# Performance work log

Hardware: AMD Instinct MI355X
Metric: run time of the kernel (lower is better)

The kernel has to match this reference:

```python
import jax, jax.numpy as jnp
import numpy as np


def setup_inputs() -> dict:
    key = jax.random.key(0)
    k1, k2, k3, k4 = jax.random.split(key, 4)
    N, F_in, F_out = 8192, 512, 256
    inp = jax.random.normal(k1, (N, F_in), dtype=jnp.float32)
    adj = jax.random.uniform(k2, (N, N), dtype=jnp.float32)
    stdv = 1.0 / np.sqrt(F_out)
    weight = jax.random.uniform(k3, (F_in, F_out), minval=-stdv, maxval=stdv, dtype=jnp.float32)
    b = jax.random.uniform(k4, (F_out,), minval=-stdv, maxval=stdv, dtype=jnp.float32)
    return {"input": inp, "adj": adj, "weight": weight, "b": b}


def reference(input, adj, weight, b):
    N = adj.shape[0]
    degree = jnp.sum(adj, axis=1)                      # [N]
    # A_tilde = 2*I - adj
    A_tilde = 2.0 * jnp.eye(N, dtype=adj.dtype) - adj
    d_inv_sqrt = 1.0 / jnp.sqrt(2.0 + degree)          # [N]
    # D^-1/2 @ A_tilde @ D^-1/2 as broadcasted row/col scaling (same math, O(N^2))
    L_sharpen = d_inv_sqrt[:, None] * A_tilde * d_inv_sqrt[None, :]
    support = input @ weight                           # [N, F_out]
    out = L_sharpen @ support + b                      # [N, F_out]
    return jax.nn.relu(out)
```

## Files before the change

kernel.cpp:

```cpp
#include <hip/hip_runtime.h>


typedef _Float16 h4 __attribute__((ext_vector_type(4)));
typedef _Float16 h8 __attribute__((ext_vector_type(8)));
typedef float f4 __attribute__((ext_vector_type(4)));

__device__ __forceinline__ void gload_lds16(const void* g, void* l) {
    __builtin_amdgcn_global_load_lds(
        (const __attribute__((address_space(1))) void*)g,
        (__attribute__((address_space(3))) void*)l, 16, 0, 0);
}

__device__ __forceinline__ void gload2(const float* p, f4& x, f4& y) {
    asm volatile("global_load_dwordx4 %0, %2, off\n\t"
                 "global_load_dwordx4 %1, %2, off offset:16"
                 : "=&v"(x), "=&v"(y)
                 : "v"(p)
                 : "memory");
}
__device__ __forceinline__ void gloadBfrag(const char* p, h8& x, h8& y) {
    asm volatile("global_load_dwordx4 %0, %2, off\n\t"
                 "global_load_dwordx4 %1, %2, off offset:1024"
                 : "=&v"(x), "=&v"(y)
                 : "v"(p)
                 : "memory");
}

__global__ __launch_bounds__(256) void k0_wt(const float* __restrict__ weight,
                                             char* __restrict__ wt) {
    const int idx = blockIdx.x * 256 + threadIdx.x;
    const int k = idx >> 8, j = idx & 255;
    const _Float16 h = (_Float16)weight[idx];
    const int off = j * 1024 + ((k >> 6) << 7) + (((k & 63) << 1) ^ ((j & 7) << 4));
    *(_Float16*)(wt + off) = h;
}

__global__ __launch_bounds__(256) void k1_deg(const float* __restrict__ adj,
                                              float* __restrict__ dinv) {
    const int r = blockIdx.x;
    const float4* rp = (const float4*)(adj + (size_t)r * 8192);
    const int t = threadIdx.x;
    float s = 0.f;
#pragma unroll
    for (int i = 0; i < 8; ++i) {
        float4 v = rp[t + i * 256];
        s += (v.x + v.y) + (v.z + v.w);
    }
#pragma unroll
    for (int off = 32; off > 0; off >>= 1) s += __shfl_down(s, off, 64);
    __shared__ float part[4];
    if ((t & 63) == 0) part[t >> 6] = s;
    __syncthreads();
    if (t == 0) {
        float deg = (part[0] + part[1]) + (part[2] + part[3]);
        dinv[r] = 1.0f / sqrtf(2.0f + deg);
    }
}

__global__ __launch_bounds__(512) void k2_support(const float* __restrict__ input,
                                                  const char* __restrict__ wt,
                                                  const float* __restrict__ dinv,
                                                  char* __restrict__ sT) {
    __shared__ char smem[4096 + 32768];
    const int t = threadIdx.x, w = t >> 6, l = t & 63;
    const int r0 = (int)blockIdx.x * 32;
    const int arow = t >> 4, ak4 = t & 15;
    const int bj = l >> 3, bb = (l & 7) * 16;

    f4 acc[2][2] = {};

    for (int kt = 0; kt < 8; ++kt) {
        const int k0 = kt * 64;
        __syncthreads();
        {
            float4 v = *(const float4*)(input + (size_t)(r0 + arow) * 512 + k0 + ak4 * 4);
            h4 h;
            h[0] = (_Float16)v.x; h[1] = (_Float16)v.y;
            h[2] = (_Float16)v.z; h[3] = (_Float16)v.w;
            *(h4*)(smem + arow * 128 + ((ak4 * 8) ^ ((arow & 7) << 4))) = h;
        }
#pragma unroll
        for (int q = 0; q < 4; ++q) {
            const int c = q * 8 + w;
            gload_lds16(wt + (size_t)(c * 8 + bj) * 1024 + kt * 128 + bb,
                        smem + 4096 + c * 1024);
        }
        __syncthreads();
#pragma unroll
        for (int kk = 0; kk < 2; ++kk) {
            const int ko = kk * 64 + ((l >> 4) << 4);
            h8 a[2], b[2];
#pragma unroll
            for (int m = 0; m < 2; ++m) {
                const int r = m * 16 + (l & 15);
                a[m] = *(const h8*)(smem + r * 128 + (ko ^ ((r & 7) << 4)));
            }
#pragma unroll
            for (int n = 0; n < 2; ++n) {
                const int j = w * 32 + n * 16 + (l & 15);
                b[n] = *(const h8*)(smem + 4096 + j * 128 + (ko ^ ((j & 7) << 4)));
            }
#pragma unroll
            for (int m = 0; m < 2; ++m)
#pragma unroll
                for (int n = 0; n < 2; ++n)
                    acc[m][n] = __builtin_amdgcn_mfma_f32_16x16x32_f16(a[m], b[n], acc[m][n], 0, 0, 0);
        }
    }
#pragma unroll
    for (int m = 0; m < 2; ++m)
#pragma unroll
        for (int n = 0; n < 2; ++n) {
            const int j = w * 32 + n * 16 + (l & 15);
            const int k0r = r0 + m * 16 + ((l >> 4) << 2);
            h4 h;
#pragma unroll
            for (int r = 0; r < 4; ++r)
                h[r] = (_Float16)(dinv[k0r + r] * acc[m][n][r]);
            const int off = (((j >> 4) * 128 + (k0r >> 6)) << 11) +
                            (((k0r >> 5) & 1) << 10) +
                            ((((k0r >> 3) & 3) << 4) + (j & 15)) * 16 +
                            ((k0r & 7) << 1);
            *(h4*)(sT + off) = h;
        }
}

__global__ __launch_bounds__(512, 4) void k3_spmm(const float* __restrict__ adj,
                                                  const char* __restrict__ sT,
                                                  float* __restrict__ part,
                                                  float* __restrict__ out,
                                                  int steps) {
    __shared__ __align__(16) char smem[2][8192];
    const int t = threadIdx.x;
    const int w = t >> 6, l = t & 63;
    const int i0 = (int)blockIdx.x * 64;
    const int ks0 = (int)blockIdx.y * steps * 64;
    const int dkt = (i0 - ks0) >> 6;

    const int arow = t >> 3;
    const int ak8 = (t & 7) * 8;
    const int arow_g = i0 + arow;
    const float* aptr = adj + (size_t)arow_g * 8192 + ks0 + ak8;
    const int a_off = arow * 128 + (((t & 7) << 4) ^ ((arow & 7) << 4));

    const int chunk0 = ks0 >> 6;
    const char* bpn0 = sT + ((size_t)(w * 2) * 128 + chunk0) * 2048 + l * 16;
    const char* bpn1 = bpn0 + 262144;

    f4 acc[4][2] = {};
    h8 bvA[2][2], bvB[2][2];
    f4 ax0, ay0, ax1, ay1;

    auto loadB = [&](int kt, h8 (&bv)[2][2]) {
        gloadBfrag(bpn0 + (size_t)kt * 2048, bv[0][0], bv[1][0]);
        gloadBfrag(bpn1 + (size_t)kt * 2048, bv[0][1], bv[1][1]);
    };
    auto writeA = [&](char* buf, int kt, const f4 x, const f4 y) {
        const int kg = ks0 + kt * 64 + ak8;
        h8 h;
        if (kt == dkt) {
#pragma unroll
            for (int e = 0; e < 4; ++e)
                h[e] = (_Float16)((arow_g == kg + e) ? 2.0f - x[e] : -x[e]);
#pragma unroll
            for (int e = 0; e < 4; ++e)
                h[4 + e] = (_Float16)((arow_g == kg + 4 + e) ? 2.0f - y[e] : -y[e]);
        } else {
#pragma unroll
            for (int e = 0; e < 4; ++e) h[e] = (_Float16)(-x[e]);
#pragma unroll
            for (int e = 0; e < 4; ++e) h[4 + e] = (_Float16)(-y[e]);
        }
        *(h8*)(buf + a_off) = h;
    };
    auto compute = [&](const char* A, const h8 (&bv)[2][2]) {
#pragma unroll
        for (int kk = 0; kk < 2; ++kk) {
            const int ko = kk * 64 + ((l >> 4) << 4);
            h8 a[4];
#pragma unroll
            for (int m = 0; m < 4; ++m) {
                const int r = m * 16 + (l & 15);
                a[m] = *(const h8*)(A + r * 128 + (ko ^ ((r & 7) << 4)));
            }
#pragma unroll
            for (int m = 0; m < 4; ++m)
#pragma unroll
                for (int n = 0; n < 2; ++n)
                    acc[m][n] = __builtin_amdgcn_mfma_f32_16x16x32_f16(a[m], bv[kk][n], acc[m][n], 0, 0, 0);
        }
    };

#define SBAR0() __builtin_amdgcn_sched_barrier(0)
#define WAIT_ADJ(N, X, Y)                                                     \
    asm volatile("s_waitcnt vmcnt(" #N ")" : "+v"(X), "+v"(Y) :: "memory");   \
    SBAR0();
#define WAIT_STEP(N, X, Y, BV)                                                \
    asm volatile("s_waitcnt vmcnt(" #N ")"                                    \
                 : "+v"(X), "+v"(Y), "+v"(BV[0][0]), "+v"(BV[0][1]),          \
                   "+v"(BV[1][0]), "+v"(BV[1][1]) :: "memory");               \
    SBAR0();
#define WAIT_BV(N, BV)                                                        \
    asm volatile("s_waitcnt vmcnt(" #N ")"                                    \
                 : "+v"(BV[0][0]), "+v"(BV[0][1]),                            \
                   "+v"(BV[1][0]), "+v"(BV[1][1]) :: "memory");               \
    SBAR0();
#define BARRIER()                                                             \
    asm volatile("s_waitcnt lgkmcnt(0)\n\ts_barrier" ::: "memory");           \
    SBAR0();

    gload2(aptr, ax0, ay0);
    loadB(0, bvA);
    WAIT_ADJ(4, ax0, ay0)
    writeA(smem[0], 0, ax0, ay0);
    gload2(aptr + 64, ax1, ay1);
    BARRIER()

#define BODY(kt, XC, YC, XN, YN, BVC, BVN, BUFC, BUFN)                        \
    {                                                                         \
        loadB((kt) + 1, BVN);                                                 \
        gload2(aptr + (size_t)((kt) + 2) * 64, XC, YC);                       \
        WAIT_STEP(6, XN, YN, BVC)                                             \
        writeA(BUFN, (kt) + 1, XN, YN);                                       \
        compute(BUFC, BVC);                                                   \
        BARRIER()                                                             \
    }

    for (int kt2 = 0; kt2 + 2 <= steps - 2; kt2 += 2) {
        BODY(kt2,     ax0, ay0, ax1, ay1, bvA, bvB, smem[0], smem[1])
        BODY(kt2 + 1, ax1, ay1, ax0, ay0, bvB, bvA, smem[1], smem[0])
    }
    {
        loadB(steps - 1, bvB);
        WAIT_STEP(4, ax1, ay1, bvA)
        writeA(smem[1], steps - 1, ax1, ay1);
        compute(smem[0], bvA);
        BARRIER()
    }
    {
        WAIT_BV(0, bvB)
        compute(smem[1], bvB);
    }
#undef BODY
#undef WAIT_ADJ
#undef WAIT_STEP
#undef WAIT_BV
#undef BARRIER
#undef SBAR0

    float* dst = (blockIdx.y == gridDim.y - 1) ? out
               : part + (size_t)blockIdx.y * (8192 * 256);
#pragma unroll
    for (int m = 0; m < 4; ++m)
#pragma unroll
        for (int n = 0; n < 2; ++n) {
            const int j = w * 32 + n * 16 + (l & 15);
            const int ib = i0 + m * 16 + ((l >> 4) << 2);
#pragma unroll
            for (int r = 0; r < 4; ++r)
                dst[(size_t)(ib + r) * 256 + j] = acc[m][n][r];
        }
}

__global__ __launch_bounds__(256) void k4_fin(const float* __restrict__ part,
                                              float* __restrict__ out,
                                              const float* __restrict__ dinv,
                                              const float* __restrict__ bias,
                                              int nsplit) {
    const int idx = blockIdx.x * 256 + threadIdx.x;
    float4 s = ((const float4*)out)[idx];
    for (int sp = 0; sp < nsplit - 1; ++sp)
        s += ((const float4*)(part + (size_t)sp * (8192 * 256)))[idx];
    const float dv = dinv[idx >> 6];
    const float4 b = ((const float4*)bias)[idx & 63];
    float4 r;
    r.x = fmaxf(dv * s.x + b.x, 0.f);
    r.y = fmaxf(dv * s.y + b.y, 0.f);
    r.z = fmaxf(dv * s.z + b.z, 0.f);
    r.w = fmaxf(dv * s.w + b.w, 0.f);
    ((float4*)out)[idx] = r;
}

extern "C" void kernel_launch(void* const* d_in, const int* in_sizes, int n_in,
                              void* d_out, int out_size, void* d_ws, size_t ws_size,
                              hipStream_t stream) {
    const float* input  = (const float*)d_in[0];
    const float* adj    = (const float*)d_in[1];
    const float* weight = (const float*)d_in[2];
    const float* bias   = (const float*)d_in[3];
    float* out = (float*)d_out;

    char* ws = (char*)d_ws;
    float* dinv = (float*)ws;
    char*  wt   = ws + 32768;
    char*  sT   = ws + 294912;
    float* part = (float*)(ws + 294912 + 4194304);

    const size_t base = 294912 + 4194304;
    int nsplit = 1;
    if (ws_size >= base + 3 * 8388608) nsplit = 4;
    else if (ws_size >= base + 1 * 8388608) nsplit = 2;
    const int steps = 128 / nsplit;

    k0_wt<<<512, 256, 0, stream>>>(weight, wt);
    k1_deg<<<8192, 256, 0, stream>>>(adj, dinv);
    k2_support<<<256, 512, 0, stream>>>(input, wt, dinv, sT);
    k3_spmm<<<dim3(128, nsplit), 512, 0, stream>>>(adj, sT, part, out, steps);
    k4_fin<<<2048, 256, 0, stream>>>(part, out, dinv, bias, nsplit);
}
```

Baseline: 136.9 us.

## Widen SpMM K-tile to 256 with four sub-steps per barrier

Restructures the k3_spmm main loop so each LDS tile covers 256 columns of adj instead of 64. Each tile is processed in four 64-wide sub-steps, with B-fragment loads double-buffered across sub-steps and the next adj tile's loads interleaved between them. The goal is to need one workgroup barrier per 256 columns rather than per 64, and to keep more global loads in flight. In exchange LDS per block grows from 16 KB to 64 KB and more registers are live, which may reduce occupancy under launch_bounds(512,4).

```diff
diff --git a/kernel.cpp b/kernel.cpp
--- a/kernel.cpp
+++ b/kernel.cpp
@@ -130,58 +130,70 @@
                                                   float* __restrict__ part,
                                                   float* __restrict__ out,
                                                   int steps) {
-    __shared__ __align__(16) char smem[2][8192];
+    __shared__ __align__(16) char smem[2][32768];
     const int t = threadIdx.x;
     const int w = t >> 6, l = t & 63;
     const int i0 = (int)blockIdx.x * 64;
-    const int ks0 = (int)blockIdx.y * steps * 64;
-    const int dkt = (i0 - ks0) >> 6;
+    const int ks0 = (int)blockIdx.y * steps * 256;
+    const int ts_d = ((unsigned)(i0 - ks0) < (unsigned)(steps * 256))
+                     ? ((i0 - ks0) >> 8) : -1;
 
     const int arow = t >> 3;
-    const int ak8 = (t & 7) * 8;
+    const int ak16 = (t & 7) * 16;
     const int arow_g = i0 + arow;
-    const float* aptr = adj + (size_t)arow_g * 8192 + ks0 + ak8;
-    const int a_off = arow * 128 + (((t & 7) << 4) ^ ((arow & 7) << 4));
-
-    const int chunk0 = ks0 >> 6;
-    const char* bpn0 = sT + ((size_t)(w * 2) * 128 + chunk0) * 2048 + l * 16;
+    const float* aptr = adj + (size_t)arow_g * 8192 + ks0 + ak16;
+    const int aswz = (arow & 7) << 4;
+    const int abase = arow * 512;
+
+    const char* bpn0 = sT + ((size_t)(w * 2) * 128 + (ks0 >> 6)) * 2048 + l * 16;
     const char* bpn1 = bpn0 + 262144;
 
     f4 acc[4][2] = {};
     h8 bvA[2][2], bvB[2][2];
-    f4 ax0, ay0, ax1, ay1;
-
-    auto loadB = [&](int kt, h8 (&bv)[2][2]) {
-        gloadBfrag(bpn0 + (size_t)kt * 2048, bv[0][0], bv[1][0]);
-        gloadBfrag(bpn1 + (size_t)kt * 2048, bv[0][1], bv[1][1]);
+    f4 pa0, pa1, pa2, pa3;
+    f4 pb0, pb1, pb2, pb3;
+
+    auto loadB = [&](int s, h8 (&bv)[2][2]) {
+        gloadBfrag(bpn0 + (size_t)s * 2048, bv[0][0], bv[1][0]);
+        gloadBfrag(bpn1 + (size_t)s * 2048, bv[0][1], bv[1][1]);
     };
-    auto writeA = [&](char* buf, int kt, const f4 x, const f4 y) {
-        const int kg = ks0 + kt * 64 + ak8;
-        h8 h;
-        if (kt == dkt) {
-#pragma unroll
-            for (int e = 0; e < 4; ++e)
-                h[e] = (_Float16)((arow_g == kg + e) ? 2.0f - x[e] : -x[e]);
-#pragma unroll
-            for (int e = 0; e < 4; ++e)
-                h[4 + e] = (_Float16)((arow_g == kg + 4 + e) ? 2.0f - y[e] : -y[e]);
+    auto loadAr = [&](int tile, int r, f4& x0, f4& y0, f4& x1, f4& y1) {
+        const float* p = aptr + (size_t)tile * 256 + r * 128;
+        gload2(p, x0, y0);
+        gload2(p + 8, x1, y1);
+    };
+    auto writeAr = [&](char* buf, int tile, int r,
+                       const f4 x0, const f4 y0, const f4 x1, const f4 y1) {
+        h8 u, v;
+        if (tile == ts_d) {
+            const int kg = ks0 + tile * 256 + ak16 + r * 128;
+#pragma unroll
+            for (int e = 0; e < 4; ++e) {
+                u[e]     = (_Float16)((arow_g == kg + e     ) ? 2.0f - x0[e] : -x0[e]);
+                u[4 + e] = (_Float16)((arow_g == kg + 4 + e ) ? 2.0f - y0[e] : -y0[e]);
+                v[e]     = (_Float16)((arow_g == kg + 8 + e ) ? 2.0f - x1[e] : -x1[e]);
+                v[4 + e] = (_Float16)((arow_g == kg + 12 + e) ? 2.0f - y1[e] : -y1[e]);
+            }
         } else {
 #pragma unroll
-            for (int e = 0; e < 4; ++e) h[e] = (_Float16)(-x[e]);
-#pragma unroll
-            for (int e = 0; e < 4; ++e) h[4 + e] = (_Float16)(-y[e]);
-        }
-        *(h8*)(buf + a_off) = h;
+            for (int e = 0; e < 4; ++e) {
+                u[e] = (_Float16)(-x0[e]); u[4 + e] = (_Float16)(-y0[e]);
+                v[e] = (_Float16)(-x1[e]); v[4 + e] = (_Float16)(-y1[e]);
+            }
+        }
+        const int kb = (ak16 << 1) + r * 256;
+        *(h8*)(buf + abase + (kb ^ aswz)) = u;
+        *(h8*)(buf + abase + ((kb + 16) ^ aswz)) = v;
     };
-    auto compute = [&](const char* A, const h8 (&bv)[2][2]) {
+    auto compute = [&](const char* A, int sp, const h8 (&bv)[2][2]) {
 #pragma unroll
         for (int kk = 0; kk < 2; ++kk) {
-            const int ko = kk * 64 + ((l >> 4) << 4);
+            const int kb = sp * 128 + kk * 64 + ((l >> 4) << 4);
             h8 a[4];
 #pragma unroll
             for (int m = 0; m < 4; ++m) {
                 const int r = m * 16 + (l & 15);
-                a[m] = *(const h8*)(A + r * 128 + (ko ^ ((r & 7) << 4)));
+                a[m] = *(const h8*)(A + r * 512 + (kb ^ ((r & 7) << 4)));
             }
 #pragma unroll
             for (int m = 0; m < 4; ++m)
@@ -192,61 +204,78 @@
     };
 
 #define SBAR0() __builtin_amdgcn_sched_barrier(0)
-#define WAIT_ADJ(N, X, Y)                                                     \
-    asm volatile("s_waitcnt vmcnt(" #N ")" : "+v"(X), "+v"(Y) :: "memory");   \
-    SBAR0();
-#define WAIT_STEP(N, X, Y, BV)                                                \
-    asm volatile("s_waitcnt vmcnt(" #N ")"                                    \
-                 : "+v"(X), "+v"(Y), "+v"(BV[0][0]), "+v"(BV[0][1]),          \
-                   "+v"(BV[1][0]), "+v"(BV[1][1]) :: "memory");               \
-    SBAR0();
 #define WAIT_BV(N, BV)                                                        \
     asm volatile("s_waitcnt vmcnt(" #N ")"                                    \
                  : "+v"(BV[0][0]), "+v"(BV[0][1]),                            \
                    "+v"(BV[1][0]), "+v"(BV[1][1]) :: "memory");               \
     SBAR0();
+#define WAIT_BVA(N, BV, X0, Y0, X1, Y1)                                       \
+    asm volatile("s_waitcnt vmcnt(" #N ")"                                    \
+                 : "+v"(BV[0][0]), "+v"(BV[0][1]),                            \
+                   "+v"(BV[1][0]), "+v"(BV[1][1]),                            \
+                   "+v"(X0), "+v"(Y0), "+v"(X1), "+v"(Y1) :: "memory");       \
+    SBAR0();
 #define BARRIER()                                                             \
     asm volatile("s_waitcnt lgkmcnt(0)\n\ts_barrier" ::: "memory");           \
     SBAR0();
 
-    gload2(aptr, ax0, ay0);
+    loadAr(0, 0, pa0, pa1, pa2, pa3);
+    loadAr(0, 1, pb0, pb1, pb2, pb3);
     loadB(0, bvA);
-    WAIT_ADJ(4, ax0, ay0)
-    writeA(smem[0], 0, ax0, ay0);
-    gload2(aptr + 64, ax1, ay1);
+    asm volatile("s_waitcnt vmcnt(8)"
+                 : "+v"(pa0), "+v"(pa1), "+v"(pa2), "+v"(pa3) :: "memory");
+    SBAR0();
+    writeAr(smem[0], 0, 0, pa0, pa1, pa2, pa3);
+    asm volatile("s_waitcnt vmcnt(4)"
+                 : "+v"(pb0), "+v"(pb1), "+v"(pb2), "+v"(pb3) :: "memory");
+    SBAR0();
+    writeAr(smem[0], 0, 1, pb0, pb1, pb2, pb3);
     BARRIER()
 
-#define BODY(kt, XC, YC, XN, YN, BVC, BVN, BUFC, BUFN)                        \
-    {                                                                         \
-        loadB((kt) + 1, BVN);                                                 \
-        gload2(aptr + (size_t)((kt) + 2) * 64, XC, YC);                       \
-        WAIT_STEP(6, XN, YN, BVC)                                             \
-        writeA(BUFN, (kt) + 1, XN, YN);                                       \
-        compute(BUFC, BVC);                                                   \
-        BARRIER()                                                             \
-    }
-
-    for (int kt2 = 0; kt2 + 2 <= steps - 2; kt2 += 2) {
-        BODY(kt2,     ax0, ay0, ax1, ay1, bvA, bvB, smem[0], smem[1])
-        BODY(kt2 + 1, ax1, ay1, ax0, ay0, bvB, bvA, smem[1], smem[0])
+    for (int ts = 0; ts + 1 < steps; ++ts) {
+        char* AC = smem[ts & 1];
+        char* AN = smem[(ts & 1) ^ 1];
+        const int s0 = ts * 4;
+        loadB(s0 + 1, bvB);
+        WAIT_BV(4, bvA)
+        compute(AC, 0, bvA);
+
+        loadB(s0 + 2, bvA);
+        loadAr(ts + 1, 0, pa0, pa1, pa2, pa3);
+        WAIT_BV(8, bvB)
+        compute(AC, 1, bvB);
+
+        loadB(s0 + 3, bvB);
+        WAIT_BVA(4, bvA, pa0, pa1, pa2, pa3)
+        writeAr(AN, ts + 1, 0, pa0, pa1, pa2, pa3);
+        loadAr(ts + 1, 1, pb0, pb1, pb2, pb3);
+        compute(AC, 2, bvA);
+
+        loadB(s0 + 4, bvA);
+        WAIT_BVA(4, bvB, pb0, pb1, pb2, pb3)
+        writeAr(AN, ts + 1, 1, pb0, pb1, pb2, pb3);
+        compute(AC, 3, bvB);
+        BARRIER()
     }
     {
-        loadB(steps - 1, bvB);
-        WAIT_STEP(4, ax1, ay1, bvA)
-        writeA(smem[1], steps - 1, ax1, ay1);
-        compute(smem[0], bvA);
-        BARRIER()
-    }
-    {
+        const char* AC = smem[(steps - 1) & 1];
+        const int s0 = (steps - 1) * 4;
+        loadB(s0 + 1, bvB);
+        WAIT_BV(4, bvA)
+        compute(AC, 0, bvA);
+        loadB(s0 + 2, bvA);
+        WAIT_BV(4, bvB)
+        compute(AC, 1, bvB);
+        loadB(s0 + 3, bvB);
+        WAIT_BV(4, bvA)
+        compute(AC, 2, bvA);
         WAIT_BV(0, bvB)
-        compute(smem[1], bvB);
-    }
-#undef BODY
-#undef WAIT_ADJ
-#undef WAIT_STEP
+        compute(AC, 3, bvB);
+    }
+#undef SBAR0
 #undef WAIT_BV
+#undef WAIT_BVA
 #undef BARRIER
-#undef SBAR0
 
     float* dst = (blockIdx.y == gridDim.y - 1) ? out
                : part + (size_t)blockIdx.y * (8192 * 256);
@@ -300,7 +329,7 @@
     int nsplit = 1;
     if (ws_size >= base + 3 * 8388608) nsplit = 4;
     else if (ws_size >= base + 1 * 8388608) nsplit = 2;
-    const int steps = 128 / nsplit;
+    const int steps = 8192 / (nsplit * 256);
 
     k0_wt<<<512, 256, 0, stream>>>(weight, wt);
     k1_deg<<<8192, 256, 0, stream>>>(adj, dinv);
```

New measurement: 138.4 us. No clear change (+1.1%).

## Fuse split-K finalize into spmm via atomic counter and restructure degree kernel

Applied to the files above, without the earlier changes.

Removes the separate finalize kernel. Every split-K block of the spmm kernel now writes its partial sums to a workspace slot, bumps a per-row-tile atomic counter, and the last block to arrive sums all slots with cache-bypassing loads and applies the dinv scale, bias and ReLU. The degree kernel is rewritten so each half-wavefront handles one row, with 16 rows per block and 4 independent accumulators, to cut block count and reduction overhead. In exchange every split slot (including the last) is written out and then read back, and the workspace check changes so that only 4-way split or no split is selected.

```diff
diff --git a/kernel.cpp b/kernel.cpp
--- a/kernel.cpp
+++ b/kernel.cpp
@@ -10,51 +10,57 @@
         (const __attribute__((address_space(1))) void*)g,
         (__attribute__((address_space(3))) void*)l, 16, 0, 0);
 }
-
 __device__ __forceinline__ void gload2(const float* p, f4& x, f4& y) {
     asm volatile("global_load_dwordx4 %0, %2, off\n\t"
                  "global_load_dwordx4 %1, %2, off offset:16"
-                 : "=&v"(x), "=&v"(y)
-                 : "v"(p)
-                 : "memory");
+                 : "=&v"(x), "=&v"(y) : "v"(p) : "memory");
 }
 __device__ __forceinline__ void gloadBfrag(const char* p, h8& x, h8& y) {
     asm volatile("global_load_dwordx4 %0, %2, off\n\t"
                  "global_load_dwordx4 %1, %2, off offset:1024"
-                 : "=&v"(x), "=&v"(y)
-                 : "v"(p)
-                 : "memory");
+                 : "=&v"(x), "=&v"(y) : "v"(p) : "memory");
+}
+__device__ __forceinline__ f4 gloadSC(const float* p) {
+    f4 v;
+    asm volatile("global_load_dwordx4 %0, %1, off sc0 sc1\n\t"
+                 "s_waitcnt vmcnt(0)"
+                 : "=v"(v) : "v"(p) : "memory");
+    return v;
 }
 
 __global__ __launch_bounds__(256) void k0_wt(const float* __restrict__ weight,
-                                             char* __restrict__ wt) {
+                                             char* __restrict__ wt,
+                                             int* __restrict__ cnt) {
     const int idx = blockIdx.x * 256 + threadIdx.x;
     const int k = idx >> 8, j = idx & 255;
     const _Float16 h = (_Float16)weight[idx];
     const int off = j * 1024 + ((k >> 6) << 7) + (((k & 63) << 1) ^ ((j & 7) << 4));
     *(_Float16*)(wt + off) = h;
-}
-
-__global__ __launch_bounds__(256) void k1_deg(const float* __restrict__ adj,
+    if (blockIdx.x == 0 && threadIdx.x < 128) cnt[threadIdx.x] = 0;
+}
+
+__global__ __launch_bounds__(512) void k1_deg(const float* __restrict__ adj,
                                               float* __restrict__ dinv) {
-    const int r = blockIdx.x;
-    const float4* rp = (const float4*)(adj + (size_t)r * 8192);
     const int t = threadIdx.x;
-    float s = 0.f;
-#pragma unroll
-    for (int i = 0; i < 8; ++i) {
-        float4 v = rp[t + i * 256];
-        s += (v.x + v.y) + (v.z + v.w);
-    }
-#pragma unroll
-    for (int off = 32; off > 0; off >>= 1) s += __shfl_down(s, off, 64);
-    __shared__ float part[4];
-    if ((t & 63) == 0) part[t >> 6] = s;
-    __syncthreads();
-    if (t == 0) {
-        float deg = (part[0] + part[1]) + (part[2] + part[3]);
-        dinv[r] = 1.0f / sqrtf(2.0f + deg);
-    }
+    const int w = t >> 6, l = t & 63, l32 = l & 31;
+    const int row = (int)blockIdx.x * 16 + w * 2 + (l >> 5);
+    const float4* rp = (const float4*)(adj + (size_t)row * 8192);
+    float a0 = 0.f, a1 = 0.f, a2 = 0.f, a3 = 0.f;
+#pragma unroll 4
+    for (int i = 0; i < 16; ++i) {
+        float4 v0 = rp[l32 + 32 * (4 * i)];
+        float4 v1 = rp[l32 + 32 * (4 * i + 1)];
+        float4 v2 = rp[l32 + 32 * (4 * i + 2)];
+        float4 v3 = rp[l32 + 32 * (4 * i + 3)];
+        a0 += (v0.x + v0.y) + (v0.z + v0.w);
+        a1 += (v1.x + v1.y) + (v1.z + v1.w);
+        a2 += (v2.x + v2.y) + (v2.z + v2.w);
+        a3 += (v3.x + v3.y) + (v3.z + v3.w);
+    }
+    float s = (a0 + a1) + (a2 + a3);
+#pragma unroll
+    for (int m = 16; m > 0; m >>= 1) s += __shfl_xor(s, m, 64);
+    if (l32 == 0) dinv[row] = 1.0f / sqrtf(2.0f + s);
 }
 
 __global__ __launch_bounds__(512) void k2_support(const float* __restrict__ input,
@@ -129,12 +135,17 @@
                                                   const char* __restrict__ sT,
                                                   float* __restrict__ part,
                                                   float* __restrict__ out,
-                                                  int steps) {
+                                                  const float* __restrict__ dinv,
+                                                  const float* __restrict__ bias,
+                                                  int* __restrict__ cnt,
+                                                  int steps, int nsplit) {
     __shared__ __align__(16) char smem[2][8192];
+    __shared__ int sflag;
     const int t = threadIdx.x;
     const int w = t >> 6, l = t & 63;
-    const int i0 = (int)blockIdx.x * 64;
-    const int ks0 = (int)blockIdx.y * steps * 64;
+    const int bx = (int)blockIdx.x, by = (int)blockIdx.y;
+    const int i0 = bx * 64;
+    const int ks0 = by * steps * 64;
     const int dkt = (i0 - ks0) >> 6;
 
     const int arow = t >> 3;
@@ -143,8 +154,7 @@
     const float* aptr = adj + (size_t)arow_g * 8192 + ks0 + ak8;
     const int a_off = arow * 128 + (((t & 7) << 4) ^ ((arow & 7) << 4));
 
-    const int chunk0 = ks0 >> 6;
-    const char* bpn0 = sT + ((size_t)(w * 2) * 128 + chunk0) * 2048 + l * 16;
+    const char* bpn0 = sT + ((size_t)(w * 2) * 128 + (ks0 >> 6)) * 2048 + l * 16;
     const char* bpn1 = bpn0 + 262144;
 
     f4 acc[4][2] = {};
@@ -248,8 +258,7 @@
 #undef BARRIER
 #undef SBAR0
 
-    float* dst = (blockIdx.y == gridDim.y - 1) ? out
-               : part + (size_t)blockIdx.y * (8192 * 256);
+    float* pslot = part + (size_t)by * (8192 * 256);
 #pragma unroll
     for (int m = 0; m < 4; ++m)
 #pragma unroll
@@ -258,27 +267,30 @@
             const int ib = i0 + m * 16 + ((l >> 4) << 2);
 #pragma unroll
             for (int r = 0; r < 4; ++r)
-                dst[(size_t)(ib + r) * 256 + j] = acc[m][n][r];
-        }
-}
-
-__global__ __launch_bounds__(256) void k4_fin(const float* __restrict__ part,
-                                              float* __restrict__ out,
-                                              const float* __restrict__ dinv,
-                                              const float* __restrict__ bias,
-                                              int nsplit) {
-    const int idx = blockIdx.x * 256 + threadIdx.x;
-    float4 s = ((const float4*)out)[idx];
-    for (int sp = 0; sp < nsplit - 1; ++sp)
-        s += ((const float4*)(part + (size_t)sp * (8192 * 256)))[idx];
-    const float dv = dinv[idx >> 6];
-    const float4 b = ((const float4*)bias)[idx & 63];
-    float4 r;
-    r.x = fmaxf(dv * s.x + b.x, 0.f);
-    r.y = fmaxf(dv * s.y + b.y, 0.f);
-    r.z = fmaxf(dv * s.z + b.z, 0.f);
-    r.w = fmaxf(dv * s.w + b.w, 0.f);
-    ((float4*)out)[idx] = r;
+                pslot[(size_t)(ib + r) * 256 + j] = acc[m][n][r];
+        }
+    __threadfence();
+    __syncthreads();
+    if (t == 0) sflag = atomicAdd(&cnt[bx], 1);
+    __syncthreads();
+    if (sflag == nsplit - 1) {
+#pragma unroll 2
+        for (int q = 0; q < 8; ++q) {
+            const int idx = q * 512 + t;
+            const size_t off = (size_t)i0 * 256 + (size_t)idx * 4;
+            f4 s = {0.f, 0.f, 0.f, 0.f};
+            for (int sp = 0; sp < nsplit; ++sp)
+                s += gloadSC(part + (size_t)sp * (8192 * 256) + off);
+            const float dv = dinv[i0 + (idx >> 6)];
+            const float4 b = ((const float4*)bias)[idx & 63];
+            float4 r;
+            r.x = fmaxf(dv * s[0] + b.x, 0.f);
+            r.y = fmaxf(dv * s[1] + b.y, 0.f);
+            r.z = fmaxf(dv * s[2] + b.z, 0.f);
+            r.w = fmaxf(dv * s[3] + b.w, 0.f);
+            ((float4*)out)[(size_t)i0 * 64 + idx] = r;
+        }
+    }
 }
 
 extern "C" void kernel_launch(void* const* d_in, const int* in_sizes, int n_in,
@@ -295,16 +307,15 @@
     char*  wt   = ws + 32768;
     char*  sT   = ws + 294912;
     float* part = (float*)(ws + 294912 + 4194304);
-
-    const size_t base = 294912 + 4194304;
-    int nsplit = 1;
-    if (ws_size >= base + 3 * 8388608) nsplit = 4;
-    else if (ws_size >= base + 1 * 8388608) nsplit = 2;
+    int*   cnt  = (int*)(ws + 294912 + 4194304 + 4ull * 8388608);
+
+    const size_t need4 = 294912 + 4194304 + 4ull * 8388608 + 512;
+    const int nsplit = (ws_size >= need4) ? 4 : 1;
     const int steps = 128 / nsplit;
 
-    k0_wt<<<512, 256, 0, stream>>>(weight, wt);
-    k1_deg<<<8192, 256, 0, stream>>>(adj, dinv);
+    k0_wt<<<512, 256, 0, stream>>>(weight, wt, cnt);
+    k1_deg<<<512, 512, 0, stream>>>(adj, dinv);
     k2_support<<<256, 512, 0, stream>>>(input, wt, dinv, sT);
-    k3_spmm<<<dim3(128, nsplit), 512, 0, stream>>>(adj, sT, part, out, steps);
-    k4_fin<<<2048, 256, 0, stream>>>(part, out, dinv, bias, nsplit);
-}
+    k3_spmm<<<dim3(128, nsplit), 512, 0, stream>>>(adj, sT, part, out,
+                                                   dinv, bias, cnt, steps, nsplit);
+}
```

Measured after the change: 328.6 us. 2.4x slower.
